# Performance work log

Hardware: AMD Instinct MI355X
Metric: run time of the kernel (lower is better)

## Reference

```python
import jax, jax.numpy as jnp
import numpy as np

N = 50000   # nodes
E = 800000  # edges
F = 128     # num_features
H = 128     # n_hidden_channels
C = 16      # num_classes


def _gcn_conv(x, W, b, src, dst, dinv):
    """PyG GCNConv: h = x @ W; out = D^-1/2 (A+I) D^-1/2 h + b."""
    h = x @ W                                   # [N, out]
    coef = dinv[src] * dinv[dst]                # [E]
    msg = h[src] * coef[:, None]                # gather + scale
    agg = jax.ops.segment_sum(msg, dst, num_segments=N)
    agg = agg + h * (dinv * dinv)[:, None]      # self-loop term
    return agg + b


def setup_inputs() -> dict:
    key = jax.random.key(0)
    ks = jax.random.split(key, 8)
    x = jax.random.normal(ks[0], (N, F), dtype=jnp.float32)
    edge_index = jax.random.randint(ks[1], (2, E), 0, N, dtype=jnp.int64)

    def glorot(k, fan_in, fan_out):
        return jax.random.normal(k, (fan_in, fan_out), dtype=jnp.float32) / np.sqrt(fan_in)

    return {
        "x": x,
        "edge_index": edge_index,
        "W1": glorot(ks[2], F, H), "b1": jnp.zeros((H,), jnp.float32),
        "W2": glorot(ks[3], H, H), "b2": jnp.zeros((H,), jnp.float32),
        "W3": glorot(ks[4], H, H), "b3": jnp.zeros((H,), jnp.float32),
        "W4": glorot(ks[5], H, C), "b4": jnp.zeros((C,), jnp.float32),
        "Wc": glorot(ks[6], C, 1), "bc": jnp.zeros((1,), jnp.float32),
    }


def reference(x, edge_index, W1, b1, W2, b2, W3, b3, W4, b4, Wc, bc):
    src, dst = edge_index[0], edge_index[1]
    # degree with self-loops (edge_weight = 1)
    deg = jax.ops.segment_sum(jnp.ones((E,), x.dtype), dst, num_segments=N) + 1.0
    dinv = jax.lax.rsqrt(deg)

    out = _gcn_conv(x, W1, b1, src, dst, dinv)
    out = jnp.tanh(_gcn_conv(out, W2, b2, src, dst, dinv))
    out = jax.nn.leaky_relu(_gcn_conv(out, W3, b3, src, dst, dinv), negative_slope=0.01)
    out = jax.nn.leaky_relu(_gcn_conv(out, W4, b4, src, dst, dinv), negative_slope=0.01)
    out = jax.nn.elu(out @ Wc + bc)             # [N, 1]
    return out
```

## Files before the change

kernel.cpp:

```cpp
#include <hip/hip_runtime.h>
#include <hip/hip_bf16.h>
#include <cstdint>
#include <cstddef>

#define NN 50000
#define NE 800000

using short8v = __attribute__((ext_vector_type(8))) short;
using f32x4 = __attribute__((ext_vector_type(4))) float;

__device__ __forceinline__ unsigned short f2bf(float f) {
    unsigned u = __float_as_uint(f);
    u += 0x7fffu + ((u >> 16) & 1u);
    return (unsigned short)(u >> 16);
}
__device__ __forceinline__ float bf2f(unsigned s) {
    return __uint_as_float(s << 16);
}


__global__ __launch_bounds__(256) void count_deg_rank(const int* __restrict__ dst,
                                                      int* __restrict__ cntP,
                                                      int* __restrict__ rank, int E) {
    int e = blockIdx.x * 256 + threadIdx.x;
    if (e < E) {
        int d = dst[e];
        rank[e] = atomicAdd(&cntP[d << 4], 1);
    }
}

__global__ __launch_bounds__(1024) void scan1(const int* __restrict__ cntP,
                                              int* __restrict__ local,
                                              int* __restrict__ bsum,
                                              float* __restrict__ dinv, int N) {
    int t = threadIdx.x;
    int g = blockIdx.x * 1024 + t;
    int lane = t & 63, w = t >> 6;
    int v = (g < N) ? cntP[g << 4] : 0;
    if (g < N) dinv[g] = rsqrtf((float)v + 1.0f);
    int x = v;
    #pragma unroll
    for (int off = 1; off < 64; off <<= 1) {
        int y = __shfl_up(x, off);
        if (lane >= off) x += y;
    }
    __shared__ int wsum[16];
    if (lane == 63) wsum[w] = x;
    __syncthreads();
    if (t < 16) {
        int s = wsum[t];
        int xx = s;
        #pragma unroll
        for (int off = 1; off < 16; off <<= 1) {
            int y = __shfl_up(xx, off);
            if (t >= off) xx += y;
        }
        wsum[t] = xx - s;
    }
    __syncthreads();
    int excl = wsum[w] + x - v;
    if (g < N) local[g] = excl;
    if (t == 1023) bsum[blockIdx.x] = excl + v;
}

__global__ __launch_bounds__(256) void scan3(const int* __restrict__ local,
                                             const int* __restrict__ bsum,
                                             int* __restrict__ rowptr,
                                             int N, int E, int NB) {
    __shared__ int sb[64];
    int t = threadIdx.x;
    if (t < 64) {
        int v = (t < NB) ? bsum[t] : 0;
        int x = v;
        #pragma unroll
        for (int off = 1; off < 64; off <<= 1) {
            int y = __shfl_up(x, off);
            if (t >= off) x += y;
        }
        sb[t] = x - v;
    }
    __syncthreads();
    int g = blockIdx.x * 256 + t;
    if (g < N) rowptr[g] = local[g] + sb[g >> 10];
    if (g == 0) rowptr[N] = E;
}

__global__ __launch_bounds__(256) void scatter_split(const int* __restrict__ src,
                                                     const int* __restrict__ dst,
                                                     const int* __restrict__ rowptr,
                                                     const int* __restrict__ rank,
                                                     int* __restrict__ csr, int E,
                                                     int sblocks,
                                                     const float* __restrict__ Wa,
                                                     const float* __restrict__ Wb,
                                                     const float* __restrict__ Wc,
                                                     unsigned short* __restrict__ WTh,
                                                     unsigned short* __restrict__ WTl) {
    if ((int)blockIdx.x < sblocks) {
        int e = blockIdx.x * 256 + threadIdx.x;
        if (e < E) {
            int d = dst[e];
            csr[rowptr[d] + rank[e]] = src[e];
        }
    } else {
        int i = (blockIdx.x - sblocks) * 256 + threadIdx.x;
        int j = i >> 14;
        int idx = i & 16383;
        int n = idx >> 7, k = idx & 127;
        const float* W = (j == 0) ? Wa : (j == 1) ? Wb : Wc;
        float v = W[k * 128 + n];
        unsigned short h = f2bf(v);
        WTh[i] = h;
        WTl[i] = f2bf(v - bf2f(h));
    }
}


template <bool F32IN>
__global__ __launch_bounds__(256) void gemm_mfma(const void* __restrict__ Xin,
                                                 const void* __restrict__ Xlin,
                                                 const unsigned short* __restrict__ WTh,
                                                 const unsigned short* __restrict__ WTl,
                                                 const float* __restrict__ dinv,
                                                 float* __restrict__ out, int N) {
    __shared__ unsigned short xh[64 * 128];
    __shared__ unsigned short xl[64 * 128];
    __shared__ unsigned short wh[128 * 40];
    __shared__ unsigned short wl[128 * 40];
    int tid = threadIdx.x;
    int lane = tid & 63, wv = tid >> 6;
    int row0 = blockIdx.x * 64;

    #pragma unroll
    for (int i = 0; i < 4; ++i) {
        int id = i * 256 + tid;
        int r = id >> 4, kc = id & 15;
        uint4 vh = make_uint4(0, 0, 0, 0), vl = make_uint4(0, 0, 0, 0);
        if (row0 + r < N) {
            if constexpr (F32IN) {
                const float* Xf = (const float*)Xin;
                float4 a = *(const float4*)(Xf + (size_t)(row0 + r) * 128 + kc * 8);
                float4 b = *(const float4*)(Xf + (size_t)(row0 + r) * 128 + kc * 8 + 4);
                unsigned short h0 = f2bf(a.x), h1 = f2bf(a.y), h2 = f2bf(a.z), h3 = f2bf(a.w);
                unsigned short h4 = f2bf(b.x), h5 = f2bf(b.y), h6 = f2bf(b.z), h7 = f2bf(b.w);
                vh = make_uint4((unsigned)h0 | ((unsigned)h1 << 16),
                                (unsigned)h2 | ((unsigned)h3 << 16),
                                (unsigned)h4 | ((unsigned)h5 << 16),
                                (unsigned)h6 | ((unsigned)h7 << 16));
                vl = make_uint4((unsigned)f2bf(a.x - bf2f(h0)) | ((unsigned)f2bf(a.y - bf2f(h1)) << 16),
                                (unsigned)f2bf(a.z - bf2f(h2)) | ((unsigned)f2bf(a.w - bf2f(h3)) << 16),
                                (unsigned)f2bf(b.x - bf2f(h4)) | ((unsigned)f2bf(b.y - bf2f(h5)) << 16),
                                (unsigned)f2bf(b.z - bf2f(h6)) | ((unsigned)f2bf(b.w - bf2f(h7)) << 16));
            } else {
                vh = *(const uint4*)&((const unsigned*)Xin)[(size_t)(row0 + r) * 64 + kc * 4];
                vl = *(const uint4*)&((const unsigned*)Xlin)[(size_t)(row0 + r) * 64 + kc * 4];
            }
        }
        int off = r * 128 + ((kc * 8) ^ ((r & 7) << 3));
        *(uint4*)&xh[off] = vh;
        *(uint4*)&xl[off] = vl;
    }

    int mstrip = (wv & 1) * 32;
    int nbase = (wv >> 1) * 64;
    f32x4 acc[2][4] = {};

    for (int ks = 0; ks < 4; ++ks) {
        __syncthreads();
        #pragma unroll
        for (int i = 0; i < 2; ++i) {
            int id = i * 256 + tid;
            int n = id >> 2, q = id & 3;
            *(uint4*)&wh[n * 40 + q * 8] =
                *(const uint4*)&WTh[(size_t)n * 128 + ks * 32 + q * 8];
            *(uint4*)&wl[n * 40 + q * 8] =
                *(const uint4*)&WTl[(size_t)n * 128 + ks * 32 + q * 8];
        }
        __syncthreads();

        short8v afh[2], afl[2];
        #pragma unroll
        for (int mt = 0; mt < 2; ++mt) {
            int r = mstrip + mt * 16 + (lane & 15);
            int off = r * 128 + ((ks * 32 + ((lane >> 4) * 8)) ^ ((r & 7) << 3));
            afh[mt] = *(const short8v*)&xh[off];
            afl[mt] = *(const short8v*)&xl[off];
        }
        #pragma unroll
        for (int nt = 0; nt < 4; ++nt) {
            int c = nbase + nt * 16 + (lane & 15);
            int boff = c * 40 + (lane >> 4) * 8;
            short8v bfh = *(const short8v*)&wh[boff];
            short8v bfl = *(const short8v*)&wl[boff];
            #pragma unroll
            for (int mt = 0; mt < 2; ++mt) {
                acc[mt][nt] = __builtin_amdgcn_mfma_f32_16x16x32_bf16(afh[mt], bfh, acc[mt][nt], 0, 0, 0);
                acc[mt][nt] = __builtin_amdgcn_mfma_f32_16x16x32_bf16(afh[mt], bfl, acc[mt][nt], 0, 0, 0);
                acc[mt][nt] = __builtin_amdgcn_mfma_f32_16x16x32_bf16(afl[mt], bfh, acc[mt][nt], 0, 0, 0);
            }
        }
    }

    #pragma unroll
    for (int mt = 0; mt < 2; ++mt) {
        #pragma unroll
        for (int i = 0; i < 4; ++i) {
            int r = row0 + mstrip + mt * 16 + (lane >> 4) * 4 + i;
            if (r < N) {
                float dv = dinv[r];
                #pragma unroll
                for (int nt = 0; nt < 4; ++nt) {
                    int cg = nbase + nt * 16 + (lane & 15);
                    out[(size_t)r * 128 + cg] = acc[mt][nt][i] * dv;
                }
            }
        }
    }
}

__global__ __launch_bounds__(256) void gemm16(const unsigned* __restrict__ Xh,
                                              const unsigned* __restrict__ Xl,
                                              const float* __restrict__ W,
                                              const float* __restrict__ dinv,
                                              float* __restrict__ out, int N) {
    __shared__ float xs[64][128];
    __shared__ float ws4[128][16];
    int tid = threadIdx.x;
    int row0 = blockIdx.x * 64;

    #pragma unroll
    for (int i = 0; i < 2; ++i)
        ((float4*)ws4)[i * 256 + tid] = ((const float4*)W)[i * 256 + tid];

    #pragma unroll
    for (int i = 0; i < 8; ++i) {
        int id = i * 256 + tid;
        int r = id >> 5, c4 = id & 31;
        float4 v = make_float4(0.f, 0.f, 0.f, 0.f);
        if (row0 + r < N) {
            uint2 hh = *(const uint2*)&Xh[(size_t)(row0 + r) * 64 + c4 * 2];
            uint2 ll = *(const uint2*)&Xl[(size_t)(row0 + r) * 64 + c4 * 2];
            v.x = bf2f(hh.x & 0xffffu) + bf2f(ll.x & 0xffffu);
            v.y = bf2f(hh.x >> 16) + bf2f(ll.x >> 16);
            v.z = bf2f(hh.y & 0xffffu) + bf2f(ll.y & 0xffffu);
            v.w = bf2f(hh.y >> 16) + bf2f(ll.y >> 16);
        }
        *(float4*)&xs[r][c4 * 4] = v;
    }
    __syncthreads();

    int ty = tid >> 4, tx = tid & 15;
    float acc[4] = {};
    #pragma unroll 4
    for (int k = 0; k < 128; ++k) {
        float wvv = ws4[k][tx];
        #pragma unroll
        for (int i = 0; i < 4; ++i)
            acc[i] = fmaf(xs[ty * 4 + i][k], wvv, acc[i]);
    }
    #pragma unroll
    for (int i = 0; i < 4; ++i) {
        int r = row0 + ty * 4 + i;
        if (r < N) out[(size_t)r * 16 + tx] = acc[i] * dinv[r];
    }
}


template <int ACT>
__global__ __launch_bounds__(256) void agg128(const float* __restrict__ HS,
                                              const int* __restrict__ rp,
                                              const int* __restrict__ csr,
                                              const float* __restrict__ dinv,
                                              const float* __restrict__ b,
                                              unsigned* __restrict__ Xh,
                                              unsigned* __restrict__ Xl, int N) {
    int wid = threadIdx.x >> 6, lane = threadIdx.x & 63;
    int n = blockIdx.x * 4 + wid;
    if (n >= N) return;
    const float2* H2 = (const float2*)HS;
    float2 a0 = H2[(size_t)n * 64 + lane];
    float2 a1 = make_float2(0.f, 0.f), a2 = a1, a3 = a1;
    float2 a4 = a1, a5 = a1, a6 = a1, a7 = a1;
    int e = rp[n], end = rp[n + 1];
    for (; e + 8 <= end; e += 8) {
        int s0 = csr[e], s1 = csr[e + 1], s2 = csr[e + 2], s3 = csr[e + 3];
        int s4 = csr[e + 4], s5 = csr[e + 5], s6 = csr[e + 6], s7 = csr[e + 7];
        float2 v0 = H2[(size_t)s0 * 64 + lane];
        float2 v1 = H2[(size_t)s1 * 64 + lane];
        float2 v2 = H2[(size_t)s2 * 64 + lane];
        float2 v3 = H2[(size_t)s3 * 64 + lane];
        float2 v4 = H2[(size_t)s4 * 64 + lane];
        float2 v5 = H2[(size_t)s5 * 64 + lane];
        float2 v6 = H2[(size_t)s6 * 64 + lane];
        float2 v7 = H2[(size_t)s7 * 64 + lane];
        a0.x += v0.x; a0.y += v0.y; a1.x += v1.x; a1.y += v1.y;
        a2.x += v2.x; a2.y += v2.y; a3.x += v3.x; a3.y += v3.y;
        a4.x += v4.x; a4.y += v4.y; a5.x += v5.x; a5.y += v5.y;
        a6.x += v6.x; a6.y += v6.y; a7.x += v7.x; a7.y += v7.y;
    }
    if (e + 4 <= end) {
        int s0 = csr[e], s1 = csr[e + 1], s2 = csr[e + 2], s3 = csr[e + 3];
        float2 v0 = H2[(size_t)s0 * 64 + lane];
        float2 v1 = H2[(size_t)s1 * 64 + lane];
        float2 v2 = H2[(size_t)s2 * 64 + lane];
        float2 v3 = H2[(size_t)s3 * 64 + lane];
        a4.x += v0.x; a4.y += v0.y; a5.x += v1.x; a5.y += v1.y;
        a6.x += v2.x; a6.y += v2.y; a7.x += v3.x; a7.y += v3.y;
        e += 4;
    }
    for (; e < end; ++e) {
        int s = csr[e];
        float2 v = H2[(size_t)s * 64 + lane];
        a0.x += v.x; a0.y += v.y;
    }
    float accx = ((a0.x + a1.x) + (a2.x + a3.x)) + ((a4.x + a5.x) + (a6.x + a7.x));
    float accy = ((a0.y + a1.y) + (a2.y + a3.y)) + ((a4.y + a5.y) + (a6.y + a7.y));
    float dv = dinv[n];
    float2 bb = ((const float2*)b)[lane];
    float ox = fmaf(dv, accx, bb.x);
    float oy = fmaf(dv, accy, bb.y);
    if (ACT == 1) { ox = tanhf(ox); oy = tanhf(oy); }
    else if (ACT == 2) {
        ox = ox > 0.f ? ox : 0.01f * ox;
        oy = oy > 0.f ? oy : 0.01f * oy;
    }
    unsigned short h0 = f2bf(ox), h1 = f2bf(oy);
    float l0 = ox - bf2f(h0), l1 = oy - bf2f(h1);
    Xh[(size_t)n * 64 + lane] = (unsigned)h0 | ((unsigned)h1 << 16);
    Xl[(size_t)n * 64 + lane] = (unsigned)f2bf(l0) | ((unsigned)f2bf(l1) << 16);
}


__global__ __launch_bounds__(256) void final_layer(const float* __restrict__ HS4,
                                                   const int* __restrict__ rp,
                                                   const int* __restrict__ csr,
                                                   const float* __restrict__ dinv,
                                                   const float* __restrict__ b4,
                                                   const float* __restrict__ Wc,
                                                   const float* __restrict__ bc,
                                                   float* __restrict__ out, int N) {
    int wid = threadIdx.x >> 6, lane = threadIdx.x & 63;
    int n = blockIdx.x * 4 + wid;
    if (n >= N) return;
    int f = lane & 15, g = lane >> 4;
    float acc = 0.f;
    int beg = rp[n], end = rp[n + 1];
    for (int e = beg + g; e < end; e += 4)
        acc += HS4[(size_t)csr[e] * 16 + f];
    acc += __shfl_xor(acc, 16);
    acc += __shfl_xor(acc, 32);
    acc += HS4[(size_t)n * 16 + f];
    float t = fmaf(dinv[n], acc, b4[f]);
    t = t > 0.f ? t : 0.01f * t;
    float p = t * Wc[f];
    p += __shfl_xor(p, 1);
    p += __shfl_xor(p, 2);
    p += __shfl_xor(p, 4);
    p += __shfl_xor(p, 8);
    if (lane == 0) {
        float z = p + bc[0];
        out[n] = z > 0.f ? z : expm1f(z);
    }
}


extern "C" void kernel_launch(void* const* d_in, const int* in_sizes, int n_in,
                              void* d_out, int out_size, void* d_ws, size_t ws_size,
                              hipStream_t stream) {
    const int N = NN, E = NE;
    const float* x  = (const float*)d_in[0];
    const int*   ei = (const int*)d_in[1];
    const float* W1 = (const float*)d_in[2];
    const float* b1 = (const float*)d_in[3];
    const float* W2 = (const float*)d_in[4];
    const float* b2 = (const float*)d_in[5];
    const float* W3 = (const float*)d_in[6];
    const float* b3 = (const float*)d_in[7];
    const float* W4 = (const float*)d_in[8];
    const float* b4 = (const float*)d_in[9];
    const float* Wc = (const float*)d_in[10];
    const float* bc = (const float*)d_in[11];
    float* out = (float*)d_out;
    const int* src = ei;
    const int* dst = ei + E;

    char* p = (char*)d_ws;
    auto carve = [&](size_t bytes) -> char* {
        char* q = p;
        p += (bytes + 255) & ~(size_t)255;
        return q;
    };
    int*            cntP   = (int*)carve((size_t)N * 16 * 4);
    int*            rank   = (int*)carve((size_t)E * 4);
    int*            rowptr = (int*)carve((size_t)(N + 1) * 4);
    float*          dinv   = (float*)carve((size_t)N * 4);
    int*            csr    = (int*)carve((size_t)E * 4);
    int*            locsc  = (int*)carve((size_t)N * 4);
    int*            bsum   = (int*)carve((size_t)64 * 4);
    unsigned short* WTh    = (unsigned short*)carve((size_t)3 * 16384 * 2);
    unsigned short* WTl    = (unsigned short*)carve((size_t)3 * 16384 * 2);
    unsigned*       Xh     = (unsigned*)carve((size_t)N * 64 * 4);
    unsigned*       Xl     = (unsigned*)carve((size_t)N * 64 * 4);
    float*          bufB   = (float*)carve((size_t)N * 128 * 4);

    const int NB = (N + 1023) / 1024;
    const int sblocks = (E + 255) / 256;
    const int wblocks = (3 * 16384) / 256;

    hipMemsetAsync(cntP, 0, (size_t)N * 16 * 4, stream);
    count_deg_rank<<<sblocks, 256, 0, stream>>>(dst, cntP, rank, E);
    scan1<<<NB, 1024, 0, stream>>>(cntP, locsc, bsum, dinv, N);
    scan3<<<(N + 255) / 256, 256, 0, stream>>>(locsc, bsum, rowptr, N, E, NB);
    scatter_split<<<sblocks + wblocks, 256, 0, stream>>>(src, dst, rowptr, rank, csr, E,
                                                         sblocks, W1, W2, W3, WTh, WTl);

    int gblocks = (N + 63) / 64;
    int ablocks = (N + 3) / 4;

    gemm_mfma<true><<<gblocks, 256, 0, stream>>>(x, nullptr, WTh, WTl, dinv, bufB, N);
    agg128<0><<<ablocks, 256, 0, stream>>>(bufB, rowptr, csr, dinv, b1, Xh, Xl, N);
    gemm_mfma<false><<<gblocks, 256, 0, stream>>>(Xh, Xl, WTh + 16384, WTl + 16384, dinv, bufB, N);
    agg128<1><<<ablocks, 256, 0, stream>>>(bufB, rowptr, csr, dinv, b2, Xh, Xl, N);
    gemm_mfma<false><<<gblocks, 256, 0, stream>>>(Xh, Xl, WTh + 32768, WTl + 32768, dinv, bufB, N);
    agg128<2><<<ablocks, 256, 0, stream>>>(bufB, rowptr, csr, dinv, b3, Xh, Xl, N);
    gemm16<<<gblocks, 256, 0, stream>>>(Xh, Xl, W4, dinv, bufB, N);
    final_layer<<<ablocks, 256, 0, stream>>>(bufB, rowptr, csr, dinv, b4, Wc, bc, out, N);
}
```

Before: 330.8 us.

## Fuse neighbor aggregation with next layer GEMM and read weights from global

```diff
diff --git a/kernel.cpp b/kernel.cpp
--- a/kernel.cpp
+++ b/kernel.cpp
@@ -94,6 +94,7 @@
                                                      const float* __restrict__ Wa,
                                                      const float* __restrict__ Wb,
                                                      const float* __restrict__ Wc,
+                                                     const float* __restrict__ Wd,
                                                      unsigned short* __restrict__ WTh,
                                                      unsigned short* __restrict__ WTl) {
     if ((int)blockIdx.x < sblocks) {
@@ -104,11 +105,18 @@
         }
     } else {
         int i = (blockIdx.x - sblocks) * 256 + threadIdx.x;
-        int j = i >> 14;
-        int idx = i & 16383;
-        int n = idx >> 7, k = idx & 127;
-        const float* W = (j == 0) ? Wa : (j == 1) ? Wb : Wc;
-        float v = W[k * 128 + n];
+        float v;
+        if (i < 49152) {
+            int j = i >> 14;
+            int idx = i & 16383;
+            int n = idx >> 7, k = idx & 127;
+            const float* W = (j == 0) ? Wa : (j == 1) ? Wb : Wc;
+            v = W[k * 128 + n];
+        } else {
+            int idx = i - 49152;
+            int n = idx >> 7, k = idx & 127;
+            v = Wd[k * 16 + n];
+        }
         unsigned short h = f2bf(v);
         WTh[i] = h;
         WTl[i] = f2bf(v - bf2f(h));
@@ -116,17 +124,13 @@
 }
 
 
-template <bool F32IN>
-__global__ __launch_bounds__(256) void gemm_mfma(const void* __restrict__ Xin,
-                                                 const void* __restrict__ Xlin,
-                                                 const unsigned short* __restrict__ WTh,
-                                                 const unsigned short* __restrict__ WTl,
-                                                 const float* __restrict__ dinv,
-                                                 float* __restrict__ out, int N) {
+__global__ __launch_bounds__(256) void gemm_l1(const float* __restrict__ Xf,
+                                               const unsigned short* __restrict__ WTh,
+                                               const unsigned short* __restrict__ WTl,
+                                               const float* __restrict__ dinv,
+                                               float* __restrict__ out, int N) {
     __shared__ unsigned short xh[64 * 128];
     __shared__ unsigned short xl[64 * 128];
-    __shared__ unsigned short wh[128 * 40];
-    __shared__ unsigned short wl[128 * 40];
     int tid = threadIdx.x;
     int lane = tid & 63, wv = tid >> 6;
     int row0 = blockIdx.x * 64;
@@ -137,47 +141,30 @@
         int r = id >> 4, kc = id & 15;
         uint4 vh = make_uint4(0, 0, 0, 0), vl = make_uint4(0, 0, 0, 0);
         if (row0 + r < N) {
-            if constexpr (F32IN) {
-                const float* Xf = (const float*)Xin;
-                float4 a = *(const float4*)(Xf + (size_t)(row0 + r) * 128 + kc * 8);
-                float4 b = *(const float4*)(Xf + (size_t)(row0 + r) * 128 + kc * 8 + 4);
-                unsigned short h0 = f2bf(a.x), h1 = f2bf(a.y), h2 = f2bf(a.z), h3 = f2bf(a.w);
-                unsigned short h4 = f2bf(b.x), h5 = f2bf(b.y), h6 = f2bf(b.z), h7 = f2bf(b.w);
-                vh = make_uint4((unsigned)h0 | ((unsigned)h1 << 16),
-                                (unsigned)h2 | ((unsigned)h3 << 16),
-                                (unsigned)h4 | ((unsigned)h5 << 16),
-                                (unsigned)h6 | ((unsigned)h7 << 16));
-                vl = make_uint4((unsigned)f2bf(a.x - bf2f(h0)) | ((unsigned)f2bf(a.y - bf2f(h1)) << 16),
-                                (unsigned)f2bf(a.z - bf2f(h2)) | ((unsigned)f2bf(a.w - bf2f(h3)) << 16),
-                                (unsigned)f2bf(b.x - bf2f(h4)) | ((unsigned)f2bf(b.y - bf2f(h5)) << 16),
-                                (unsigned)f2bf(b.z - bf2f(h6)) | ((unsigned)f2bf(b.w - bf2f(h7)) << 16));
-            } else {
-                vh = *(const uint4*)&((const unsigned*)Xin)[(size_t)(row0 + r) * 64 + kc * 4];
-                vl = *(const uint4*)&((const unsigned*)Xlin)[(size_t)(row0 + r) * 64 + kc * 4];
-            }
+            float4 a = *(const float4*)(Xf + (size_t)(row0 + r) * 128 + kc * 8);
+            float4 b = *(const float4*)(Xf + (size_t)(row0 + r) * 128 + kc * 8 + 4);
+            unsigned short h0 = f2bf(a.x), h1 = f2bf(a.y), h2 = f2bf(a.z), h3 = f2bf(a.w);
+            unsigned short h4 = f2bf(b.x), h5 = f2bf(b.y), h6 = f2bf(b.z), h7 = f2bf(b.w);
+            vh = make_uint4((unsigned)h0 | ((unsigned)h1 << 16),
+                            (unsigned)h2 | ((unsigned)h3 << 16),
+                            (unsigned)h4 | ((unsigned)h5 << 16),
+                            (unsigned)h6 | ((unsigned)h7 << 16));
+            vl = make_uint4((unsigned)f2bf(a.x - bf2f(h0)) | ((unsigned)f2bf(a.y - bf2f(h1)) << 16),
+                            (unsigned)f2bf(a.z - bf2f(h2)) | ((unsigned)f2bf(a.w - bf2f(h3)) << 16),
+                            (unsigned)f2bf(b.x - bf2f(h4)) | ((unsigned)f2bf(b.y - bf2f(h5)) << 16),
+                            (unsigned)f2bf(b.z - bf2f(h6)) | ((unsigned)f2bf(b.w - bf2f(h7)) << 16));
         }
         int off = r * 128 + ((kc * 8) ^ ((r & 7) << 3));
         *(uint4*)&xh[off] = vh;
         *(uint4*)&xl[off] = vl;
     }
+    __syncthreads();
 
     int mstrip = (wv & 1) * 32;
     int nbase = (wv >> 1) * 64;
     f32x4 acc[2][4] = {};
 
     for (int ks = 0; ks < 4; ++ks) {
-        __syncthreads();
-        #pragma unroll
-        for (int i = 0; i < 2; ++i) {
-            int id = i * 256 + tid;
-            int n = id >> 2, q = id & 3;
-            *(uint4*)&wh[n * 40 + q * 8] =
-                *(const uint4*)&WTh[(size_t)n * 128 + ks * 32 + q * 8];
-            *(uint4*)&wl[n * 40 + q * 8] =
-                *(const uint4*)&WTl[(size_t)n * 128 + ks * 32 + q * 8];
-        }
-        __syncthreads();
-
         short8v afh[2], afl[2];
         #pragma unroll
         for (int mt = 0; mt < 2; ++mt) {
@@ -189,9 +176,9 @@
         #pragma unroll
         for (int nt = 0; nt < 4; ++nt) {
             int c = nbase + nt * 16 + (lane & 15);
-            int boff = c * 40 + (lane >> 4) * 8;
-            short8v bfh = *(const short8v*)&wh[boff];
-            short8v bfl = *(const short8v*)&wl[boff];
+            size_t goff = (size_t)c * 128 + ks * 32 + (lane >> 4) * 8;
+            short8v bfh = *(const short8v*)&WTh[goff];
+            short8v bfl = *(const short8v*)&WTl[goff];
             #pragma unroll
             for (int mt = 0; mt < 2; ++mt) {
                 acc[mt][nt] = __builtin_amdgcn_mfma_f32_16x16x32_bf16(afh[mt], bfh, acc[mt][nt], 0, 0, 0);
@@ -218,116 +205,146 @@
     }
 }
 
-__global__ __launch_bounds__(256) void gemm16(const unsigned* __restrict__ Xh,
-                                              const unsigned* __restrict__ Xl,
-                                              const float* __restrict__ W,
-                                              const float* __restrict__ dinv,
-                                              float* __restrict__ out, int N) {
-    __shared__ float xs[64][128];
-    __shared__ float ws4[128][16];
-    int tid = threadIdx.x;
-    int row0 = blockIdx.x * 64;
-
-    #pragma unroll
-    for (int i = 0; i < 2; ++i)
-        ((float4*)ws4)[i * 256 + tid] = ((const float4*)W)[i * 256 + tid];
-
-    #pragma unroll
-    for (int i = 0; i < 8; ++i) {
-        int id = i * 256 + tid;
-        int r = id >> 5, c4 = id & 31;
-        float4 v = make_float4(0.f, 0.f, 0.f, 0.f);
-        if (row0 + r < N) {
-            uint2 hh = *(const uint2*)&Xh[(size_t)(row0 + r) * 64 + c4 * 2];
-            uint2 ll = *(const uint2*)&Xl[(size_t)(row0 + r) * 64 + c4 * 2];
-            v.x = bf2f(hh.x & 0xffffu) + bf2f(ll.x & 0xffffu);
-            v.y = bf2f(hh.x >> 16) + bf2f(ll.x >> 16);
-            v.z = bf2f(hh.y & 0xffffu) + bf2f(ll.y & 0xffffu);
-            v.w = bf2f(hh.y >> 16) + bf2f(ll.y >> 16);
-        }
-        *(float4*)&xs[r][c4 * 4] = v;
+
+template <int ACT, bool WIDE>
+__global__ __launch_bounds__(256) void fused_agg_gemm(
+        const float* __restrict__ HS,
+        const int* __restrict__ rp, const int* __restrict__ csr,
+        const float* __restrict__ dinv, const float* __restrict__ b,
+        const unsigned short* __restrict__ WTh,
+        const unsigned short* __restrict__ WTl,
+        float* __restrict__ out, int N) {
+    __shared__ unsigned short xh[64 * 128];
+    __shared__ unsigned short xl[64 * 128];
+    int tid = threadIdx.x, lane = tid & 63, wv = tid >> 6;
+    int base = blockIdx.x * 64;
+    const float2* H2 = (const float2*)HS;
+    float2 bb = ((const float2*)b)[lane];
+
+    for (int i = 0; i < 16; ++i) {
+        int r = wv * 16 + i;
+        int n = base + r;
+        unsigned hpack = 0, lpack = 0;
+        if (n < N) {
+            float2 a0 = H2[(size_t)n * 64 + lane];
+            float2 a1 = make_float2(0.f, 0.f), a2 = a1, a3 = a1;
+            float2 a4 = a1, a5 = a1, a6 = a1, a7 = a1;
+            int e = rp[n], end = rp[n + 1];
+            for (; e + 8 <= end; e += 8) {
+                int s0 = csr[e], s1 = csr[e + 1], s2 = csr[e + 2], s3 = csr[e + 3];
+                int s4 = csr[e + 4], s5 = csr[e + 5], s6 = csr[e + 6], s7 = csr[e + 7];
+                float2 v0 = H2[(size_t)s0 * 64 + lane];
+                float2 v1 = H2[(size_t)s1 * 64 + lane];
+                float2 v2 = H2[(size_t)s2 * 64 + lane];
+                float2 v3 = H2[(size_t)s3 * 64 + lane];
+                float2 v4 = H2[(size_t)s4 * 64 + lane];
+                float2 v5 = H2[(size_t)s5 * 64 + lane];
+                float2 v6 = H2[(size_t)s6 * 64 + lane];
+                float2 v7 = H2[(size_t)s7 * 64 + lane];
+                a0.x += v0.x; a0.y += v0.y; a1.x += v1.x; a1.y += v1.y;
+                a2.x += v2.x; a2.y += v2.y; a3.x += v3.x; a3.y += v3.y;
+                a4.x += v4.x; a4.y += v4.y; a5.x += v5.x; a5.y += v5.y;
+                a6.x += v6.x; a6.y += v6.y; a7.x += v7.x; a7.y += v7.y;
+            }
+            if (e + 4 <= end) {
+                int s0 = csr[e], s1 = csr[e + 1], s2 = csr[e + 2], s3 = csr[e + 3];
+                float2 v0 = H2[(size_t)s0 * 64 + lane];
+                float2 v1 = H2[(size_t)s1 * 64 + lane];
+                float2 v2 = H2[(size_t)s2 * 64 + lane];
+                float2 v3 = H2[(size_t)s3 * 64 + lane];
+                a4.x += v0.x; a4.y += v0.y; a5.x += v1.x; a5.y += v1.y;
+                a6.x += v2.x; a6.y += v2.y; a7.x += v3.x; a7.y += v3.y;
+                e += 4;
+            }
+            for (; e < end; ++e) {
+                int s = csr[e];
+                float2 v = H2[(size_t)s * 64 + lane];
+                a0.x += v.x; a0.y += v.y;
+            }
+            float accx = ((a0.x + a1.x) + (a2.x + a3.x)) + ((a4.x + a5.x) + (a6.x + a7.x));
+            float accy = ((a0.y + a1.y) + (a2.y + a3.y)) + ((a4.y + a5.y) + (a6.y + a7.y));
+            float dv = dinv[n];
+            float ox = fmaf(dv, accx, bb.x);
+            float oy = fmaf(dv, accy, bb.y);
+            if (ACT == 1) { ox = tanhf(ox); oy = tanhf(oy); }
+            else if (ACT == 2) {
+                ox = ox > 0.f ? ox : 0.01f * ox;
+                oy = oy > 0.f ? oy : 0.01f * oy;
+            }
+            unsigned short h0 = f2bf(ox), h1 = f2bf(oy);
+            hpack = (unsigned)h0 | ((unsigned)h1 << 16);
+            lpack = (unsigned)f2bf(ox - bf2f(h0)) | ((unsigned)f2bf(oy - bf2f(h1)) << 16);
+        }
+        int off = r * 128 + ((2 * lane) ^ ((r & 7) << 3));
+        *(unsigned*)&xh[off] = hpack;
+        *(unsigned*)&xl[off] = lpack;
     }
     __syncthreads();
 
-    int ty = tid >> 4, tx = tid & 15;
-    float acc[4] = {};
-    #pragma unroll 4
-    for (int k = 0; k < 128; ++k) {
-        float wvv = ws4[k][tx];
-        #pragma unroll
-        for (int i = 0; i < 4; ++i)
-            acc[i] = fmaf(xs[ty * 4 + i][k], wvv, acc[i]);
-    }
-    #pragma unroll
-    for (int i = 0; i < 4; ++i) {
-        int r = row0 + ty * 4 + i;
-        if (r < N) out[(size_t)r * 16 + tx] = acc[i] * dinv[r];
-    }
-}
-
-
-template <int ACT>
-__global__ __launch_bounds__(256) void agg128(const float* __restrict__ HS,
-                                              const int* __restrict__ rp,
-                                              const int* __restrict__ csr,
-                                              const float* __restrict__ dinv,
-                                              const float* __restrict__ b,
-                                              unsigned* __restrict__ Xh,
-                                              unsigned* __restrict__ Xl, int N) {
-    int wid = threadIdx.x >> 6, lane = threadIdx.x & 63;
-    int n = blockIdx.x * 4 + wid;
-    if (n >= N) return;
-    const float2* H2 = (const float2*)HS;
-    float2 a0 = H2[(size_t)n * 64 + lane];
-    float2 a1 = make_float2(0.f, 0.f), a2 = a1, a3 = a1;
-    float2 a4 = a1, a5 = a1, a6 = a1, a7 = a1;
-    int e = rp[n], end = rp[n + 1];
-    for (; e + 8 <= end; e += 8) {
-        int s0 = csr[e], s1 = csr[e + 1], s2 = csr[e + 2], s3 = csr[e + 3];
-        int s4 = csr[e + 4], s5 = csr[e + 5], s6 = csr[e + 6], s7 = csr[e + 7];
-        float2 v0 = H2[(size_t)s0 * 64 + lane];
-        float2 v1 = H2[(size_t)s1 * 64 + lane];
-        float2 v2 = H2[(size_t)s2 * 64 + lane];
-        float2 v3 = H2[(size_t)s3 * 64 + lane];
-        float2 v4 = H2[(size_t)s4 * 64 + lane];
-        float2 v5 = H2[(size_t)s5 * 64 + lane];
-        float2 v6 = H2[(size_t)s6 * 64 + lane];
-        float2 v7 = H2[(size_t)s7 * 64 + lane];
-        a0.x += v0.x; a0.y += v0.y; a1.x += v1.x; a1.y += v1.y;
-        a2.x += v2.x; a2.y += v2.y; a3.x += v3.x; a3.y += v3.y;
-        a4.x += v4.x; a4.y += v4.y; a5.x += v5.x; a5.y += v5.y;
-        a6.x += v6.x; a6.y += v6.y; a7.x += v7.x; a7.y += v7.y;
-    }
-    if (e + 4 <= end) {
-        int s0 = csr[e], s1 = csr[e + 1], s2 = csr[e + 2], s3 = csr[e + 3];
-        float2 v0 = H2[(size_t)s0 * 64 + lane];
-        float2 v1 = H2[(size_t)s1 * 64 + lane];
-        float2 v2 = H2[(size_t)s2 * 64 + lane];
-        float2 v3 = H2[(size_t)s3 * 64 + lane];
-        a4.x += v0.x; a4.y += v0.y; a5.x += v1.x; a5.y += v1.y;
-        a6.x += v2.x; a6.y += v2.y; a7.x += v3.x; a7.y += v3.y;
-        e += 4;
-    }
-    for (; e < end; ++e) {
-        int s = csr[e];
-        float2 v = H2[(size_t)s * 64 + lane];
-        a0.x += v.x; a0.y += v.y;
-    }
-    float accx = ((a0.x + a1.x) + (a2.x + a3.x)) + ((a4.x + a5.x) + (a6.x + a7.x));
-    float accy = ((a0.y + a1.y) + (a2.y + a3.y)) + ((a4.y + a5.y) + (a6.y + a7.y));
-    float dv = dinv[n];
-    float2 bb = ((const float2*)b)[lane];
-    float ox = fmaf(dv, accx, bb.x);
-    float oy = fmaf(dv, accy, bb.y);
-    if (ACT == 1) { ox = tanhf(ox); oy = tanhf(oy); }
-    else if (ACT == 2) {
-        ox = ox > 0.f ? ox : 0.01f * ox;
-        oy = oy > 0.f ? oy : 0.01f * oy;
-    }
-    unsigned short h0 = f2bf(ox), h1 = f2bf(oy);
-    float l0 = ox - bf2f(h0), l1 = oy - bf2f(h1);
-    Xh[(size_t)n * 64 + lane] = (unsigned)h0 | ((unsigned)h1 << 16);
-    Xl[(size_t)n * 64 + lane] = (unsigned)f2bf(l0) | ((unsigned)f2bf(l1) << 16);
+    if (WIDE) {
+        int mstrip = (wv & 1) * 32;
+        int nbase = (wv >> 1) * 64;
+        f32x4 acc[2][4] = {};
+        for (int ks = 0; ks < 4; ++ks) {
+            short8v afh[2], afl[2];
+            #pragma unroll
+            for (int mt = 0; mt < 2; ++mt) {
+                int r = mstrip + mt * 16 + (lane & 15);
+                int off = r * 128 + ((ks * 32 + ((lane >> 4) * 8)) ^ ((r & 7) << 3));
+                afh[mt] = *(const short8v*)&xh[off];
+                afl[mt] = *(const short8v*)&xl[off];
+            }
+            #pragma unroll
+            for (int nt = 0; nt < 4; ++nt) {
+                int c = nbase + nt * 16 + (lane & 15);
+                size_t goff = (size_t)c * 128 + ks * 32 + (lane >> 4) * 8;
+                short8v bfh = *(const short8v*)&WTh[goff];
+                short8v bfl = *(const short8v*)&WTl[goff];
+                #pragma unroll
+                for (int mt = 0; mt < 2; ++mt) {
+                    acc[mt][nt] = __builtin_amdgcn_mfma_f32_16x16x32_bf16(afh[mt], bfh, acc[mt][nt], 0, 0, 0);
+                    acc[mt][nt] = __builtin_amdgcn_mfma_f32_16x16x32_bf16(afh[mt], bfl, acc[mt][nt], 0, 0, 0);
+                    acc[mt][nt] = __builtin_amdgcn_mfma_f32_16x16x32_bf16(afl[mt], bfh, acc[mt][nt], 0, 0, 0);
+                }
+            }
+        }
+        #pragma unroll
+        for (int mt = 0; mt < 2; ++mt) {
+            #pragma unroll
+            for (int i = 0; i < 4; ++i) {
+                int r = base + mstrip + mt * 16 + (lane >> 4) * 4 + i;
+                if (r < N) {
+                    float dv = dinv[r];
+                    #pragma unroll
+                    for (int nt = 0; nt < 4; ++nt) {
+                        int cg = nbase + nt * 16 + (lane & 15);
+                        out[(size_t)r * 128 + cg] = acc[mt][nt][i] * dv;
+                    }
+                }
+            }
+        }
+    } else {
+        int mstrip = wv * 16;
+        f32x4 acc = {};
+        for (int ks = 0; ks < 4; ++ks) {
+            int r = mstrip + (lane & 15);
+            int off = r * 128 + ((ks * 32 + ((lane >> 4) * 8)) ^ ((r & 7) << 3));
+            short8v afh = *(const short8v*)&xh[off];
+            short8v afl = *(const short8v*)&xl[off];
+            int c = lane & 15;
+            size_t goff = (size_t)c * 128 + ks * 32 + (lane >> 4) * 8;
+            short8v bfh = *(const short8v*)&WTh[goff];
+            short8v bfl = *(const short8v*)&WTl[goff];
+            acc = __builtin_amdgcn_mfma_f32_16x16x32_bf16(afh, bfh, acc, 0, 0, 0);
+            acc = __builtin_amdgcn_mfma_f32_16x16x32_bf16(afh, bfl, acc, 0, 0, 0);
+            acc = __builtin_amdgcn_mfma_f32_16x16x32_bf16(afl, bfh, acc, 0, 0, 0);
+        }
+        #pragma unroll
+        for (int i = 0; i < 4; ++i) {
+            int r = base + mstrip + (lane >> 4) * 4 + i;
+            if (r < N) out[(size_t)r * 16 + (lane & 15)] = acc[i] * dinv[r];
+        }
+    }
 }
 
 
@@ -397,32 +414,32 @@
     int*            csr    = (int*)carve((size_t)E * 4);
     int*            locsc  = (int*)carve((size_t)N * 4);
     int*            bsum   = (int*)carve((size_t)64 * 4);
-    unsigned short* WTh    = (unsigned short*)carve((size_t)3 * 16384 * 2);
-    unsigned short* WTl    = (unsigned short*)carve((size_t)3 * 16384 * 2);
-    unsigned*       Xh     = (unsigned*)carve((size_t)N * 64 * 4);
-    unsigned*       Xl     = (unsigned*)carve((size_t)N * 64 * 4);
+    unsigned short* WTh    = (unsigned short*)carve((size_t)(3 * 16384 + 2048) * 2);
+    unsigned short* WTl    = (unsigned short*)carve((size_t)(3 * 16384 + 2048) * 2);
+    float*          bufA   = (float*)carve((size_t)N * 128 * 4);
     float*          bufB   = (float*)carve((size_t)N * 128 * 4);
+    float*          hs4    = (float*)carve((size_t)N * 16 * 4);
 
     const int NB = (N + 1023) / 1024;
     const int sblocks = (E + 255) / 256;
-    const int wblocks = (3 * 16384) / 256;
+    const int wblocks = (3 * 16384 + 2048) / 256;
 
     hipMemsetAsync(cntP, 0, (size_t)N * 16 * 4, stream);
     count_deg_rank<<<sblocks, 256, 0, stream>>>(dst, cntP, rank, E);
     scan1<<<NB, 1024, 0, stream>>>(cntP, locsc, bsum, dinv, N);
     scan3<<<(N + 255) / 256, 256, 0, stream>>>(locsc, bsum, rowptr, N, E, NB);
     scatter_split<<<sblocks + wblocks, 256, 0, stream>>>(src, dst, rowptr, rank, csr, E,
-                                                         sblocks, W1, W2, W3, WTh, WTl);
+                                                         sblocks, W1, W2, W3, W4, WTh, WTl);
 
     int gblocks = (N + 63) / 64;
     int ablocks = (N + 3) / 4;
 
-    gemm_mfma<true><<<gblocks, 256, 0, stream>>>(x, nullptr, WTh, WTl, dinv, bufB, N);
-    agg128<0><<<ablocks, 256, 0, stream>>>(bufB, rowptr, csr, dinv, b1, Xh, Xl, N);
-    gemm_mfma<false><<<gblocks, 256, 0, stream>>>(Xh, Xl, WTh + 16384, WTl + 16384, dinv, bufB, N);
-    agg128<1><<<ablocks, 256, 0, stream>>>(bufB, rowptr, csr, dinv, b2, Xh, Xl, N);
-    gemm_mfma<false><<<gblocks, 256, 0, stream>>>(Xh, Xl, WTh + 32768, WTl + 32768, dinv, bufB, N);
-    agg128<2><<<ablocks, 256, 0, stream>>>(bufB, rowptr, csr, dinv, b3, Xh, Xl, N);
-    gemm16<<<gblocks, 256, 0, stream>>>(Xh, Xl, W4, dinv, bufB, N);
-    final_layer<<<ablocks, 256, 0, stream>>>(bufB, rowptr, csr, dinv, b4, Wc, bc, out, N);
-}
+    gemm_l1<<<gblocks, 256, 0, stream>>>(x, WTh, WTl, dinv, bufB, N);
+    fused_agg_gemm<0, true><<<gblocks, 256, 0, stream>>>(bufB, rowptr, csr, dinv, b1,
+                                                         WTh + 16384, WTl + 16384, bufA, N);
+    fused_agg_gemm<1, true><<<gblocks, 256, 0, stream>>>(bufA, rowptr, csr, dinv, b2,
+                                                         WTh + 32768, WTl + 32768, bufB, N);
+    fused_agg_gemm<2, false><<<gblocks, 256, 0, stream>>>(bufB, rowptr, csr, dinv, b3,
+                                                          WTh + 49152, WTl + 49152, hs4, N);
+    final_layer<<<ablocks, 256, 0, stream>>>(hs4, rowptr, csr, dinv, b4, Wc, bc, out, N);
+}
```

New measurement: 344.4 us. 4.1% more time.

## Overlap first-layer GEMM with degree counting by deferring dinv scaling to aggregation

Applied to the files above, without the earlier changes.

```diff
diff --git a/kernel.cpp b/kernel.cpp
--- a/kernel.cpp
+++ b/kernel.cpp
@@ -19,15 +19,124 @@
 }
 
 
-__global__ __launch_bounds__(256) void count_deg_rank(const int* __restrict__ dst,
-                                                      int* __restrict__ cntP,
-                                                      int* __restrict__ rank, int E) {
-    int e = blockIdx.x * 256 + threadIdx.x;
-    if (e < E) {
-        int d = dst[e];
-        rank[e] = atomicAdd(&cntP[d << 4], 1);
-    }
-}
+__global__ __launch_bounds__(256) void wsplit(const float* __restrict__ Wa,
+                                              const float* __restrict__ Wb,
+                                              const float* __restrict__ Wc,
+                                              const float* __restrict__ Wd,
+                                              unsigned short* __restrict__ WTh,
+                                              unsigned short* __restrict__ WTl) {
+    int i = blockIdx.x * 256 + threadIdx.x;
+    float v;
+    if (i < 49152) {
+        int j = i >> 14;
+        int idx = i & 16383;
+        int n = idx >> 7, k = idx & 127;
+        const float* W = (j == 0) ? Wa : (j == 1) ? Wb : Wc;
+        v = W[k * 128 + n];
+    } else {
+        int idx = i - 49152;
+        int n = idx >> 7, k = idx & 127;
+        v = Wd[k * 16 + n];
+    }
+    unsigned short h = f2bf(v);
+    WTh[i] = h;
+    WTl[i] = f2bf(v - bf2f(h));
+}
+
+
+__global__ __launch_bounds__(256) void mega(const float* __restrict__ Xf,
+                                            const unsigned short* __restrict__ WTh,
+                                            const unsigned short* __restrict__ WTl,
+                                            float* __restrict__ out,
+                                            const int* __restrict__ dst,
+                                            int* __restrict__ cntP,
+                                            int* __restrict__ rank,
+                                            int N, int E, int gb) {
+    __shared__ unsigned short xh[64 * 128];
+    __shared__ unsigned short xl[64 * 128];
+    int tid = threadIdx.x;
+
+    if ((int)blockIdx.x >= gb) {
+        int e = ((int)blockIdx.x - gb) * 256 + tid;
+        if (e < E) {
+            int d = dst[e];
+            rank[e] = atomicAdd(&cntP[d << 4], 1);
+        }
+        return;
+    }
+
+    int lane = tid & 63, wv = tid >> 6;
+    int row0 = blockIdx.x * 64;
+
+    #pragma unroll
+    for (int i = 0; i < 4; ++i) {
+        int id = i * 256 + tid;
+        int r = id >> 4, kc = id & 15;
+        uint4 vh = make_uint4(0, 0, 0, 0), vl = make_uint4(0, 0, 0, 0);
+        if (row0 + r < N) {
+            float4 a = *(const float4*)(Xf + (size_t)(row0 + r) * 128 + kc * 8);
+            float4 b = *(const float4*)(Xf + (size_t)(row0 + r) * 128 + kc * 8 + 4);
+            unsigned short h0 = f2bf(a.x), h1 = f2bf(a.y), h2 = f2bf(a.z), h3 = f2bf(a.w);
+            unsigned short h4 = f2bf(b.x), h5 = f2bf(b.y), h6 = f2bf(b.z), h7 = f2bf(b.w);
+            vh = make_uint4((unsigned)h0 | ((unsigned)h1 << 16),
+                            (unsigned)h2 | ((unsigned)h3 << 16),
+                            (unsigned)h4 | ((unsigned)h5 << 16),
+                            (unsigned)h6 | ((unsigned)h7 << 16));
+            vl = make_uint4((unsigned)f2bf(a.x - bf2f(h0)) | ((unsigned)f2bf(a.y - bf2f(h1)) << 16),
+                            (unsigned)f2bf(a.z - bf2f(h2)) | ((unsigned)f2bf(a.w - bf2f(h3)) << 16),
+                            (unsigned)f2bf(b.x - bf2f(h4)) | ((unsigned)f2bf(b.y - bf2f(h5)) << 16),
+                            (unsigned)f2bf(b.z - bf2f(h6)) | ((unsigned)f2bf(b.w - bf2f(h7)) << 16));
+        }
+        int off = r * 128 + ((kc * 8) ^ ((r & 7) << 3));
+        *(uint4*)&xh[off] = vh;
+        *(uint4*)&xl[off] = vl;
+    }
+    __syncthreads();
+
+    int mstrip = (wv & 1) * 32;
+    int nbase = (wv >> 1) * 64;
+    f32x4 acc[2][4] = {};
+
+    for (int ks = 0; ks < 4; ++ks) {
+        short8v afh[2], afl[2];
+        #pragma unroll
+        for (int mt = 0; mt < 2; ++mt) {
+            int r = mstrip + mt * 16 + (lane & 15);
+            int off = r * 128 + ((ks * 32 + ((lane >> 4) * 8)) ^ ((r & 7) << 3));
+            afh[mt] = *(const short8v*)&xh[off];
+            afl[mt] = *(const short8v*)&xl[off];
+        }
+        #pragma unroll
+        for (int nt = 0; nt < 4; ++nt) {
+            int c = nbase + nt * 16 + (lane & 15);
+            size_t goff = (size_t)c * 128 + ks * 32 + (lane >> 4) * 8;
+            short8v bfh = *(const short8v*)&WTh[goff];
+            short8v bfl = *(const short8v*)&WTl[goff];
+            #pragma unroll
+            for (int mt = 0; mt < 2; ++mt) {
+                acc[mt][nt] = __builtin_amdgcn_mfma_f32_16x16x32_bf16(afh[mt], bfh, acc[mt][nt], 0, 0, 0);
+                acc[mt][nt] = __builtin_amdgcn_mfma_f32_16x16x32_bf16(afh[mt], bfl, acc[mt][nt], 0, 0, 0);
+                acc[mt][nt] = __builtin_amdgcn_mfma_f32_16x16x32_bf16(afl[mt], bfh, acc[mt][nt], 0, 0, 0);
+            }
+        }
+    }
+
+    #pragma unroll
+    for (int mt = 0; mt < 2; ++mt) {
+        #pragma unroll
+        for (int i = 0; i < 4; ++i) {
+            int r = row0 + mstrip + mt * 16 + (lane >> 4) * 4 + i;
+            if (r < N) {
+                #pragma unroll
+                for (int nt = 0; nt < 4; ++nt) {
+                    int cg = nbase + nt * 16 + (lane & 15);
+                    out[(size_t)r * 128 + cg] = acc[mt][nt][i];
+                }
+            }
+        }
+    }
+}
+
 
 __global__ __launch_bounds__(1024) void scan1(const int* __restrict__ cntP,
                                               int* __restrict__ local,
@@ -85,44 +194,25 @@
     if (g == 0) rowptr[N] = E;
 }
 
-__global__ __launch_bounds__(256) void scatter_split(const int* __restrict__ src,
+__global__ __launch_bounds__(256) void scatter_plain(const int* __restrict__ src,
                                                      const int* __restrict__ dst,
                                                      const int* __restrict__ rowptr,
                                                      const int* __restrict__ rank,
-                                                     int* __restrict__ csr, int E,
-                                                     int sblocks,
-                                                     const float* __restrict__ Wa,
-                                                     const float* __restrict__ Wb,
-                                                     const float* __restrict__ Wc,
-                                                     unsigned short* __restrict__ WTh,
-                                                     unsigned short* __restrict__ WTl) {
-    if ((int)blockIdx.x < sblocks) {
-        int e = blockIdx.x * 256 + threadIdx.x;
-        if (e < E) {
-            int d = dst[e];
-            csr[rowptr[d] + rank[e]] = src[e];
-        }
-    } else {
-        int i = (blockIdx.x - sblocks) * 256 + threadIdx.x;
-        int j = i >> 14;
-        int idx = i & 16383;
-        int n = idx >> 7, k = idx & 127;
-        const float* W = (j == 0) ? Wa : (j == 1) ? Wb : Wc;
-        float v = W[k * 128 + n];
-        unsigned short h = f2bf(v);
-        WTh[i] = h;
-        WTl[i] = f2bf(v - bf2f(h));
-    }
-}
-
-
-template <bool F32IN>
-__global__ __launch_bounds__(256) void gemm_mfma(const void* __restrict__ Xin,
-                                                 const void* __restrict__ Xlin,
-                                                 const unsigned short* __restrict__ WTh,
-                                                 const unsigned short* __restrict__ WTl,
-                                                 const float* __restrict__ dinv,
-                                                 float* __restrict__ out, int N) {
+                                                     int* __restrict__ csr, int E) {
+    int e = blockIdx.x * 256 + threadIdx.x;
+    if (e < E) {
+        int d = dst[e];
+        csr[rowptr[d] + rank[e]] = src[e];
+    }
+}
+
+
+__global__ __launch_bounds__(256) void gemm_w(const unsigned* __restrict__ Xh,
+                                              const unsigned* __restrict__ Xl,
+                                              const unsigned short* __restrict__ WTh,
+                                              const unsigned short* __restrict__ WTl,
+                                              const float* __restrict__ dinv,
+                                              float* __restrict__ out, int N) {
     __shared__ unsigned short xh[64 * 128];
     __shared__ unsigned short xl[64 * 128];
     __shared__ unsigned short wh[128 * 40];
@@ -137,24 +227,8 @@
         int r = id >> 4, kc = id & 15;
         uint4 vh = make_uint4(0, 0, 0, 0), vl = make_uint4(0, 0, 0, 0);
         if (row0 + r < N) {
-            if constexpr (F32IN) {
-                const float* Xf = (const float*)Xin;
-                float4 a = *(const float4*)(Xf + (size_t)(row0 + r) * 128 + kc * 8);
-                float4 b = *(const float4*)(Xf + (size_t)(row0 + r) * 128 + kc * 8 + 4);
-                unsigned short h0 = f2bf(a.x), h1 = f2bf(a.y), h2 = f2bf(a.z), h3 = f2bf(a.w);
-                unsigned short h4 = f2bf(b.x), h5 = f2bf(b.y), h6 = f2bf(b.z), h7 = f2bf(b.w);
-                vh = make_uint4((unsigned)h0 | ((unsigned)h1 << 16),
-                                (unsigned)h2 | ((unsigned)h3 << 16),
-                                (unsigned)h4 | ((unsigned)h5 << 16),
-                                (unsigned)h6 | ((unsigned)h7 << 16));
-                vl = make_uint4((unsigned)f2bf(a.x - bf2f(h0)) | ((unsigned)f2bf(a.y - bf2f(h1)) << 16),
-                                (unsigned)f2bf(a.z - bf2f(h2)) | ((unsigned)f2bf(a.w - bf2f(h3)) << 16),
-                                (unsigned)f2bf(b.x - bf2f(h4)) | ((unsigned)f2bf(b.y - bf2f(h5)) << 16),
-                                (unsigned)f2bf(b.z - bf2f(h6)) | ((unsigned)f2bf(b.w - bf2f(h7)) << 16));
-            } else {
-                vh = *(const uint4*)&((const unsigned*)Xin)[(size_t)(row0 + r) * 64 + kc * 4];
-                vl = *(const uint4*)&((const unsigned*)Xlin)[(size_t)(row0 + r) * 64 + kc * 4];
-            }
+            vh = *(const uint4*)&Xh[(size_t)(row0 + r) * 64 + kc * 4];
+            vl = *(const uint4*)&Xl[(size_t)(row0 + r) * 64 + kc * 4];
         }
         int off = r * 128 + ((kc * 8) ^ ((r & 7) << 3));
         *(uint4*)&xh[off] = vh;
@@ -266,7 +340,7 @@
 }
 
 
-template <int ACT>
+template <int ACT, bool DEFER>
 __global__ __launch_bounds__(256) void agg128(const float* __restrict__ HS,
                                               const int* __restrict__ rp,
                                               const int* __restrict__ csr,
@@ -278,7 +352,11 @@
     int n = blockIdx.x * 4 + wid;
     if (n >= N) return;
     const float2* H2 = (const float2*)HS;
-    float2 a0 = H2[(size_t)n * 64 + lane];
+    float dv = dinv[n];
+    float2 self = H2[(size_t)n * 64 + lane];
+    float2 a0;
+    if (DEFER) a0 = make_float2(self.x * dv, self.y * dv);
+    else       a0 = self;
     float2 a1 = make_float2(0.f, 0.f), a2 = a1, a3 = a1;
     float2 a4 = a1, a5 = a1, a6 = a1, a7 = a1;
     int e = rp[n], end = rp[n + 1];
@@ -293,10 +371,23 @@
         float2 v5 = H2[(size_t)s5 * 64 + lane];
         float2 v6 = H2[(size_t)s6 * 64 + lane];
         float2 v7 = H2[(size_t)s7 * 64 + lane];
-        a0.x += v0.x; a0.y += v0.y; a1.x += v1.x; a1.y += v1.y;
-        a2.x += v2.x; a2.y += v2.y; a3.x += v3.x; a3.y += v3.y;
-        a4.x += v4.x; a4.y += v4.y; a5.x += v5.x; a5.y += v5.y;
-        a6.x += v6.x; a6.y += v6.y; a7.x += v7.x; a7.y += v7.y;
+        if (DEFER) {
+            float d0 = dinv[s0], d1 = dinv[s1], d2 = dinv[s2], d3 = dinv[s3];
+            float d4 = dinv[s4], d5 = dinv[s5], d6 = dinv[s6], d7 = dinv[s7];
+            a0.x = fmaf(v0.x, d0, a0.x); a0.y = fmaf(v0.y, d0, a0.y);
+            a1.x = fmaf(v1.x, d1, a1.x); a1.y = fmaf(v1.y, d1, a1.y);
+            a2.x = fmaf(v2.x, d2, a2.x); a2.y = fmaf(v2.y, d2, a2.y);
+            a3.x = fmaf(v3.x, d3, a3.x); a3.y = fmaf(v3.y, d3, a3.y);
+            a4.x = fmaf(v4.x, d4, a4.x); a4.y = fmaf(v4.y, d4, a4.y);
+            a5.x = fmaf(v5.x, d5, a5.x); a5.y = fmaf(v5.y, d5, a5.y);
+            a6.x = fmaf(v6.x, d6, a6.x); a6.y = fmaf(v6.y, d6, a6.y);
+            a7.x = fmaf(v7.x, d7, a7.x); a7.y = fmaf(v7.y, d7, a7.y);
+        } else {
+            a0.x += v0.x; a0.y += v0.y; a1.x += v1.x; a1.y += v1.y;
+            a2.x += v2.x; a2.y += v2.y; a3.x += v3.x; a3.y += v3.y;
+            a4.x += v4.x; a4.y += v4.y; a5.x += v5.x; a5.y += v5.y;
+            a6.x += v6.x; a6.y += v6.y; a7.x += v7.x; a7.y += v7.y;
+        }
     }
     if (e + 4 <= end) {
         int s0 = csr[e], s1 = csr[e + 1], s2 = csr[e + 2], s3 = csr[e + 3];
@@ -304,18 +395,30 @@
         float2 v1 = H2[(size_t)s1 * 64 + lane];
         float2 v2 = H2[(size_t)s2 * 64 + lane];
         float2 v3 = H2[(size_t)s3 * 64 + lane];
-        a4.x += v0.x; a4.y += v0.y; a5.x += v1.x; a5.y += v1.y;
-        a6.x += v2.x; a6.y += v2.y; a7.x += v3.x; a7.y += v3.y;
+        if (DEFER) {
+            float d0 = dinv[s0], d1 = dinv[s1], d2 = dinv[s2], d3 = dinv[s3];
+            a4.x = fmaf(v0.x, d0, a4.x); a4.y = fmaf(v0.y, d0, a4.y);
+            a5.x = fmaf(v1.x, d1, a5.x); a5.y = fmaf(v1.y, d1, a5.y);
+            a6.x = fmaf(v2.x, d2, a6.x); a6.y = fmaf(v2.y, d2, a6.y);
+            a7.x = fmaf(v3.x, d3, a7.x); a7.y = fmaf(v3.y, d3, a7.y);
+        } else {
+            a4.x += v0.x; a4.y += v0.y; a5.x += v1.x; a5.y += v1.y;
+            a6.x += v2.x; a6.y += v2.y; a7.x += v3.x; a7.y += v3.y;
+        }
         e += 4;
     }
     for (; e < end; ++e) {
         int s = csr[e];
         float2 v = H2[(size_t)s * 64 + lane];
-        a0.x += v.x; a0.y += v.y;
+        if (DEFER) {
+            float d = dinv[s];
+            a0.x = fmaf(v.x, d, a0.x); a0.y = fmaf(v.y, d, a0.y);
+        } else {
+            a0.x += v.x; a0.y += v.y;
+        }
     }
     float accx = ((a0.x + a1.x) + (a2.x + a3.x)) + ((a4.x + a5.x) + (a6.x + a7.x));
     float accy = ((a0.y + a1.y) + (a2.y + a3.y)) + ((a4.y + a5.y) + (a6.y + a7.y));
-    float dv = dinv[n];
     float2 bb = ((const float2*)b)[lane];
     float ox = fmaf(dv, accx, bb.x);
     float oy = fmaf(dv, accy, bb.y);
@@ -397,32 +500,31 @@
     int*            csr    = (int*)carve((size_t)E * 4);
     int*            locsc  = (int*)carve((size_t)N * 4);
     int*            bsum   = (int*)carve((size_t)64 * 4);
-    unsigned short* WTh    = (unsigned short*)carve((size_t)3 * 16384 * 2);
-    unsigned short* WTl    = (unsigned short*)carve((size_t)3 * 16384 * 2);
+    unsigned short* WTh    = (unsigned short*)carve((size_t)(3 * 16384 + 2048) * 2);
+    unsigned short* WTl    = (unsigned short*)carve((size_t)(3 * 16384 + 2048) * 2);
     unsigned*       Xh     = (unsigned*)carve((size_t)N * 64 * 4);
     unsigned*       Xl     = (unsigned*)carve((size_t)N * 64 * 4);
     float*          bufB   = (float*)carve((size_t)N * 128 * 4);
+    float*          hs4    = (float*)carve((size_t)N * 16 * 4);
 
     const int NB = (N + 1023) / 1024;
-    const int sblocks = (E + 255) / 256;
-    const int wblocks = (3 * 16384) / 256;
+    const int gblocks = (N + 63) / 64;
+    const int cblocks = (E + 255) / 256;
+    const int wblocks = (3 * 16384 + 2048) / 256;
+    const int ablocks = (N + 3) / 4;
 
     hipMemsetAsync(cntP, 0, (size_t)N * 16 * 4, stream);
-    count_deg_rank<<<sblocks, 256, 0, stream>>>(dst, cntP, rank, E);
+    wsplit<<<wblocks, 256, 0, stream>>>(W1, W2, W3, W4, WTh, WTl);
+    mega<<<gblocks + cblocks, 256, 0, stream>>>(x, WTh, WTl, bufB, dst, cntP, rank, N, E, gblocks);
     scan1<<<NB, 1024, 0, stream>>>(cntP, locsc, bsum, dinv, N);
     scan3<<<(N + 255) / 256, 256, 0, stream>>>(locsc, bsum, rowptr, N, E, NB);
-    scatter_split<<<sblocks + wblocks, 256, 0, stream>>>(src, dst, rowptr, rank, csr, E,
-                                                         sblocks, W1, W2, W3, WTh, WTl);
-
-    int gblocks = (N + 63) / 64;
-    int ablocks = (N + 3) / 4;
-
-    gemm_mfma<true><<<gblocks, 256, 0, stream>>>(x, nullptr, WTh, WTl, dinv, bufB, N);
-    agg128<0><<<ablocks, 256, 0, stream>>>(bufB, rowptr, csr, dinv, b1, Xh, Xl, N);
-    gemm_mfma<false><<<gblocks, 256, 0, stream>>>(Xh, Xl, WTh + 16384, WTl + 16384, dinv, bufB, N);
-    agg128<1><<<ablocks, 256, 0, stream>>>(bufB, rowptr, csr, dinv, b2, Xh, Xl, N);
-    gemm_mfma<false><<<gblocks, 256, 0, stream>>>(Xh, Xl, WTh + 32768, WTl + 32768, dinv, bufB, N);
-    agg128<2><<<ablocks, 256, 0, stream>>>(bufB, rowptr, csr, dinv, b3, Xh, Xl, N);
-    gemm16<<<gblocks, 256, 0, stream>>>(Xh, Xl, W4, dinv, bufB, N);
-    final_layer<<<ablocks, 256, 0, stream>>>(bufB, rowptr, csr, dinv, b4, Wc, bc, out, N);
-}
+    scatter_plain<<<cblocks, 256, 0, stream>>>(src, dst, rowptr, rank, csr, E);
+
+    agg128<0, true><<<ablocks, 256, 0, stream>>>(bufB, rowptr, csr, dinv, b1, Xh, Xl, N);
+    gemm_w<<<gblocks, 256, 0, stream>>>(Xh, Xl, WTh + 16384, WTl + 16384, dinv, bufB, N);
+    agg128<1, false><<<ablocks, 256, 0, stream>>>(bufB, rowptr, csr, dinv, b2, Xh, Xl, N);
+    gemm_w<<<gblocks, 256, 0, stream>>>(Xh, Xl, WTh + 32768, WTl + 32768, dinv, bufB, N);
+    agg128<2, false><<<ablocks, 256, 0, stream>>>(bufB, rowptr, csr, dinv, b3, Xh, Xl, N);
+    gemm16<<<gblocks, 256, 0, stream>>>(Xh, Xl, W4, dinv, hs4, N);
+    final_layer<<<ablocks, 256, 0, stream>>>(hs4, rowptr, csr, dinv, b4, Wc, bc, out, N);
+}
```

After: 332.4 us. About the same (+0.5%).
